# Kernel optimization log

Measured on AMD Instinct MI355X. Metric: run time of the kernel, lower is better.

The kernel has to match this reference:

```python
import jax, jax.numpy as jnp
import numpy as np

N_HEAD = 8
NORM_GROUPS = 32
EPS = 1e-6


def setup_inputs() -> dict:
    key = jax.random.key(0)
    ks = jax.random.split(key, 9)
    B, C, H, W, D = 1, 256, 16, 16, 16
    COND = 512
    x = jax.random.normal(ks[0], (B, C, H, W, D), dtype=jnp.float32)
    cond = jax.random.normal(ks[1], (B, COND), dtype=jnp.float32)
    # AdaGN linear scale/shift (torch Linear: weight [C, cond_dim], bias [C])
    w_scale = jax.random.normal(ks[2], (C, COND), dtype=jnp.float32) * 0.02
    b_scale = jax.random.normal(ks[3], (C,), dtype=jnp.float32) * 0.02
    w_shift = jax.random.normal(ks[4], (C, COND), dtype=jnp.float32) * 0.02
    b_shift = jax.random.normal(ks[5], (C,), dtype=jnp.float32) * 0.02
    # 1x1x1 conv3d weights collapse to matrices: qkv [3C, C] (no bias), out [C, C] + bias
    w_qkv = jax.random.normal(ks[6], (3 * C, C), dtype=jnp.float32) * (1.0 / np.sqrt(C))
    w_out = jax.random.normal(ks[7], (C, C), dtype=jnp.float32) * (1.0 / np.sqrt(C))
    b_out = jax.random.normal(ks[8], (C,), dtype=jnp.float32) * 0.02
    return {"x": x, "cond": cond, "w_scale": w_scale, "b_scale": b_scale,
            "w_shift": w_shift, "b_shift": b_shift, "w_qkv": w_qkv,
            "w_out": w_out, "b_out": b_out}


def _ada_gn(x, cond, w_scale, b_scale, w_shift, b_shift):
    B, C, H, W, D = x.shape
    G = NORM_GROUPS
    xg = x.reshape(B, G, C // G, H, W, D)
    mean = jnp.mean(xg, axis=(2, 3, 4, 5), keepdims=True)
    var = jnp.var(xg, axis=(2, 3, 4, 5), keepdims=True)
    x_norm = ((xg - mean) * jax.lax.rsqrt(var + EPS)).reshape(B, C, H, W, D)
    scale = (cond @ w_scale.T + b_scale)[:, :, None, None, None]  # [B,C,1,1,1]
    shift = (cond @ w_shift.T + b_shift)[:, :, None, None, None]
    return x_norm * (1.0 + scale) + shift


def reference(x, cond, w_scale, b_scale, w_shift, b_shift, w_qkv, w_out, b_out):
    B, C, H, W, D = x.shape
    nh = N_HEAD
    hd = C // nh
    N = H * W * D  # flattened spatial tokens
    norm = _ada_gn(x, cond, w_scale, b_scale, w_shift, b_shift)
    # 1x1x1 conv == channel matmul
    qkv = jnp.einsum('oc,bchwd->bohwd', w_qkv, norm)        # [B,3C,H,W,D]
    qkv = qkv.reshape(B, nh, 3 * hd, N)
    q, k, v = jnp.split(qkv, 3, axis=2)                      # each [B,nh,hd,N]
    attn = jnp.einsum('bnci,bncj->bnij', q, k) / jnp.sqrt(jnp.float32(C))
    attn = jax.nn.softmax(attn, axis=-1)                     # [B,nh,N,N]
    out = jnp.einsum('bnij,bncj->bnci', attn, v)             # [B,nh,hd,N]
    out = out.reshape(B, C, H, W, D)
    out = jnp.einsum('oc,bchwd->bohwd', w_out, out) + b_out[None, :, None, None, None]
    return out + x
```

## Files before the change

### kernel.cpp

```cpp
#include <hip/hip_runtime.h>
#include <math.h>

#define CCH 256
#define NN  4096
#define NHEAD 8
#define CONDD 512

typedef __attribute__((ext_vector_type(8))) short short8;
typedef __attribute__((ext_vector_type(4))) float f32x4;
typedef __attribute__((ext_vector_type(16))) float f32x16;

static __device__ __forceinline__ short f2bf(float f) {
    union { float f; uint32_t u; } v; v.f = f;
    uint32_t r = v.u + 0x7fffu + ((v.u >> 16) & 1u);
    return (short)(r >> 16);
}

static __device__ __forceinline__ uint32_t cvt_pk_bf16(float a, float b) {
    uint32_t r;
    asm("v_cvt_pk_bf16_f32 %0, %1, %2" : "=v"(r) : "v"(a), "v"(b));
    return r;
}

__global__ __launch_bounds__(256) void front_fused(const float* __restrict__ x,
                                                   const float* __restrict__ cond,
                                                   const float* __restrict__ w_scale,
                                                   const float* __restrict__ b_scale,
                                                   const float* __restrict__ w_shift,
                                                   const float* __restrict__ b_shift,
                                                   const float* __restrict__ wq,
                                                   const float* __restrict__ wo,
                                                   float* __restrict__ partial,
                                                   float* __restrict__ scale,
                                                   float* __restrict__ shift,
                                                   short* __restrict__ wqb,
                                                   short* __restrict__ wob) {
    __shared__ float rs[4], rss[4];
    int bb = blockIdx.x;
    int t = threadIdx.x;
    if (bb < 256) {
        const float4* p = (const float4*)(x + bb * 4096);
        float s = 0.f, ss = 0.f;
        for (int k = t; k < 1024; k += 256) {
            float4 v = p[k];
            s += v.x + v.y + v.z + v.w;
            ss += v.x * v.x + v.y * v.y + v.z * v.z + v.w * v.w;
        }
        #pragma unroll
        for (int off = 32; off; off >>= 1) { s += __shfl_xor(s, off); ss += __shfl_xor(ss, off); }
        int wid = t >> 6;
        if ((t & 63) == 0) { rs[wid] = s; rss[wid] = ss; }
        __syncthreads();
        if (t == 0) {
            partial[2 * bb] = rs[0] + rs[1] + rs[2] + rs[3];
            partial[2 * bb + 1] = rss[0] + rss[1] + rss[2] + rss[3];
        }
    } else if (bb < 1280) {
        int idx = (bb - 256) * 256 + t;
        if (idx < 196608) wqb[idx] = f2bf(wq[idx]);
        else              wob[idx - 196608] = f2bf(wo[idx - 196608]);
    } else {
        int o = (bb - 1280) * 4 + (t >> 6);
        int lane = t & 63;
        float ds = 0.f, dh = 0.f;
        for (int k = lane; k < CONDD; k += 64) {
            float cv = cond[k];
            ds += cv * w_scale[o * CONDD + k];
            dh += cv * w_shift[o * CONDD + k];
        }
        #pragma unroll
        for (int off = 32; off; off >>= 1) { ds += __shfl_xor(ds, off); dh += __shfl_xor(dh, off); }
        if (lane == 0) { scale[o] = ds + b_scale[o]; shift[o] = dh + b_shift[o]; }
    }
}

__global__ __launch_bounds__(256) void normalize_t(const float* __restrict__ x,
                                                   const float* __restrict__ partial,
                                                   const float* __restrict__ scale,
                                                   const float* __restrict__ shift,
                                                   short* __restrict__ norm_t) {
    __shared__ float gm[8], gr[8];
    __shared__ float Aa[64], Bb[64];
    __shared__ short tile[32 * 66];
    int i0 = blockIdx.x * 32;
    int c0 = blockIdx.y * 64;
    int g0 = c0 >> 3;
    int t = threadIdx.x;
    if (t < 8) {
        float s = 0.f, ss = 0.f;
        #pragma unroll
        for (int ch = 0; ch < 8; ++ch) {
            s += partial[((g0 + t) * 8 + ch) * 2];
            ss += partial[((g0 + t) * 8 + ch) * 2 + 1];
        }
        float mean = s * (1.0f / 32768.0f);
        float var = ss * (1.0f / 32768.0f) - mean * mean;
        gm[t] = mean;
        gr[t] = rsqrtf(var + 1e-6f);
    }
    __syncthreads();
    if (t < 64) {
        int c = c0 + t;
        float a = gr[t >> 3] * (1.0f + scale[c]);
        Aa[t] = a;
        Bb[t] = shift[c] - gm[t >> 3] * a;
    }
    __syncthreads();
    #pragma unroll
    for (int e0 = 0; e0 < 8; ++e0) {
        int e = e0 * 256 + t;
        int cl = e >> 5, il = e & 31;
        float v = x[(c0 + cl) * NN + i0 + il];
        tile[il * 66 + cl] = f2bf(v * Aa[cl] + Bb[cl]);
    }
    __syncthreads();
    #pragma unroll
    for (int e0 = 0; e0 < 4; ++e0) {
        int e = e0 * 256 + t;
        int il = e >> 5, cd = e & 31;
        uint32_t d = *(const uint32_t*)&tile[il * 66 + 2 * cd];
        *(uint32_t*)&norm_t[(i0 + il) * 256 + c0 + 2 * cd] = d;
    }
}

__global__ __launch_bounds__(256) void qkv_gemm(const short* __restrict__ wqb,
                                                const short* __restrict__ norm_t,
                                                short* __restrict__ qtb, short* __restrict__ ktb,
                                                short* __restrict__ vcb) {
    int t = threadIdx.x;
    int w = t >> 6, lane = t & 63, li = lane & 15, lg = lane >> 4;
    int o0 = blockIdx.x * 32;
    int i0 = blockIdx.y * 64 + w * 16;
    f32x4 acc[2] = {{0,0,0,0},{0,0,0,0}};
    const short* bbase = norm_t + (i0 + li) * 256 + 8 * lg;
    const short* abase = wqb + (o0 + li) * 256 + 8 * lg;
    #pragma unroll
    for (int ks = 0; ks < 8; ++ks) {
        short8 bfrag = *(const short8*)(bbase + ks * 32);
        #pragma unroll
        for (int f = 0; f < 2; ++f) {
            short8 afrag = *(const short8*)(abase + f * 16 * 256 + ks * 32);
            acc[f] = __builtin_amdgcn_mfma_f32_16x16x32_bf16(afrag, bfrag, acc[f], 0, 0, 0);
        }
    }
    int i = i0 + li;
    #pragma unroll
    for (int f = 0; f < 2; ++f) {
        #pragma unroll
        for (int r = 0; r < 4; ++r) {
            int o = o0 + 16 * f + 4 * lg + r;
            float v = acc[f][r];
            int h = o / 96;
            int rr = o - h * 96;
            int cc = rr & 31;
            int kind = rr >> 5;
            if (kind == 0)      qtb[(h * NN + i) * 32 + cc] = f2bf(v * (0.0625f * 1.44269504f));
            else if (kind == 1) ktb[(h * NN + i) * 32 + cc] = f2bf(v);
            else                vcb[(h * 32 + cc) * NN + i] = f2bf(v);
        }
    }
}

union PF { uint32_t u[4]; short8 s8; };

static __device__ __forceinline__ f32x16 qk_tile(short8 k0, short8 k1, short8 qf0, short8 qf1) {
    const f32x16 z = {0,0,0,0,0,0,0,0,0,0,0,0,0,0,0,0};
    __builtin_amdgcn_s_setprio(1);
    f32x16 s = __builtin_amdgcn_mfma_f32_32x32x16_bf16(k0, qf0, z, 0, 0, 0);
    s = __builtin_amdgcn_mfma_f32_32x32x16_bf16(k1, qf1, s, 0, 0, 0);
    __builtin_amdgcn_s_setprio(0);
    return s;
}

static __device__ __forceinline__ void pv_tile(f32x16 s, short8 v0, short8 v1,
                                               f32x16& acc, float& lsum) {
    float p[16];
    #pragma unroll
    for (int r = 0; r < 16; ++r) p[r] = __builtin_amdgcn_exp2f(s[r]);
    float u0 = 0.f, u1 = 0.f;
    #pragma unroll
    for (int r = 0; r < 4; ++r) { u0 += p[r] + p[4 + r]; u1 += p[8 + r] + p[12 + r]; }
    lsum += u0 + u1;
    auto A1 = __builtin_amdgcn_permlane32_swap(cvt_pk_bf16(p[0], p[1]),   cvt_pk_bf16(p[4], p[5]),   false, false);
    auto A2 = __builtin_amdgcn_permlane32_swap(cvt_pk_bf16(p[2], p[3]),   cvt_pk_bf16(p[6], p[7]),   false, false);
    auto A3 = __builtin_amdgcn_permlane32_swap(cvt_pk_bf16(p[8], p[9]),   cvt_pk_bf16(p[12], p[13]), false, false);
    auto A4 = __builtin_amdgcn_permlane32_swap(cvt_pk_bf16(p[10], p[11]), cvt_pk_bf16(p[14], p[15]), false, false);
    PF f1, f2;
    f1.u[0] = A1[0]; f1.u[1] = A2[0]; f1.u[2] = A1[1]; f1.u[3] = A2[1];
    f2.u[0] = A3[0]; f2.u[1] = A4[0]; f2.u[2] = A3[1]; f2.u[3] = A4[1];
    __builtin_amdgcn_s_setprio(1);
    acc = __builtin_amdgcn_mfma_f32_32x32x16_bf16(v0, f1.s8, acc, 0, 0, 0);
    acc = __builtin_amdgcn_mfma_f32_32x32x16_bf16(v1, f2.s8, acc, 0, 0, 0);
    __builtin_amdgcn_s_setprio(0);
}

__global__ __launch_bounds__(256, 4) void attention_mfma(const short* __restrict__ qtb,
                                                         const short* __restrict__ ktb,
                                                         const short* __restrict__ vcb,
                                                         short* __restrict__ attnT) {
    __shared__ float lds_acc[4][32][32];
    __shared__ float lds_lsum[4][32];

    int bid = blockIdx.x;
    int h = bid & 7;
    int i_base = (bid >> 3) * 32;
    int t = threadIdx.x;
    int w = t >> 6, lane = t & 63, l31 = lane & 31, hi = lane >> 5;

    const short* qrow = qtb + (h * NN + i_base + l31) * 32;
    short8 qf0 = *(const short8*)(qrow + 8 * hi);
    short8 qf1 = *(const short8*)(qrow + 16 + 8 * hi);

    const short* kbase = ktb + (h * NN + l31) * 32 + 8 * hi;
    const short* vrow  = vcb + (h * 32 + l31) * NN + 8 * hi;

    f32x16 acc = {0,0,0,0,0,0,0,0,0,0,0,0,0,0,0,0};
    float lsum = 0.f;

    int jstart = w * 1024;
    const short* kp = kbase + jstart * 32;
    const short* vp = vrow + jstart;

    short8 k0 = *(const short8*)kp, k1 = *(const short8*)(kp + 16);
    short8 v0 = *(const short8*)vp, v1 = *(const short8*)(vp + 16);
    f32x16 sA = qk_tile(k0, k1, qf0, qf1);
    kp += 1024; k0 = *(const short8*)kp; k1 = *(const short8*)(kp + 16);
    f32x16 sB;

    #pragma unroll 1
    for (int p = 0; p < 15; ++p) {
        sB = qk_tile(k0, k1, qf0, qf1);
        kp += 1024; k0 = *(const short8*)kp; k1 = *(const short8*)(kp + 16);
        pv_tile(sA, v0, v1, acc, lsum);
        vp += 32; v0 = *(const short8*)vp; v1 = *(const short8*)(vp + 16);

        sA = qk_tile(k0, k1, qf0, qf1);
        kp += 1024; k0 = *(const short8*)kp; k1 = *(const short8*)(kp + 16);
        pv_tile(sB, v0, v1, acc, lsum);
        vp += 32; v0 = *(const short8*)vp; v1 = *(const short8*)(vp + 16);
    }
    sB = qk_tile(k0, k1, qf0, qf1);
    pv_tile(sA, v0, v1, acc, lsum);
    vp += 32; v0 = *(const short8*)vp; v1 = *(const short8*)(vp + 16);
    pv_tile(sB, v0, v1, acc, lsum);

    lsum += __shfl_xor(lsum, 32);

    #pragma unroll
    for (int r = 0; r < 16; ++r) {
        int c = (r & 3) + 8 * (r >> 2) + 4 * hi;
        lds_acc[w][c][l31] = acc[r];
    }
    if (hi == 0) lds_lsum[w][l31] = lsum;
    __syncthreads();

    int q = t & 31, c0 = (t >> 5) * 4;
    float s0 = 0.f, s1 = 0.f, s2 = 0.f, s3 = 0.f, ls = 0.f;
    #pragma unroll
    for (int ww = 0; ww < 4; ++ww) {
        s0 += lds_acc[ww][c0 + 0][q];
        s1 += lds_acc[ww][c0 + 1][q];
        s2 += lds_acc[ww][c0 + 2][q];
        s3 += lds_acc[ww][c0 + 3][q];
        ls += lds_lsum[ww][q];
    }
    float inv = 1.0f / ls;
    uint2 uu;
    uu.x = cvt_pk_bf16(s0 * inv, s1 * inv);
    uu.y = cvt_pk_bf16(s2 * inv, s3 * inv);
    *(uint2*)&attnT[(i_base + q) * 256 + h * 32 + c0] = uu;
}

__global__ __launch_bounds__(256) void proj_gemm(const short* __restrict__ wob,
                                                 const short* __restrict__ attnT,
                                                 const float* __restrict__ b_out,
                                                 const float* __restrict__ x,
                                                 float* __restrict__ out) {
    int t = threadIdx.x;
    int w = t >> 6, lane = t & 63, li = lane & 15, lg = lane >> 4;
    int o0 = blockIdx.x * 32;
    int i0 = blockIdx.y * 64 + w * 16;
    f32x4 acc[2] = {{0,0,0,0},{0,0,0,0}};
    const short* bbase = attnT + (i0 + li) * 256 + 8 * lg;
    const short* abase = wob + (o0 + li) * 256 + 8 * lg;
    #pragma unroll
    for (int ks = 0; ks < 8; ++ks) {
        short8 bfrag = *(const short8*)(bbase + ks * 32);
        #pragma unroll
        for (int f = 0; f < 2; ++f) {
            short8 afrag = *(const short8*)(abase + f * 16 * 256 + ks * 32);
            acc[f] = __builtin_amdgcn_mfma_f32_16x16x32_bf16(afrag, bfrag, acc[f], 0, 0, 0);
        }
    }
    int i = i0 + li;
    #pragma unroll
    for (int f = 0; f < 2; ++f) {
        #pragma unroll
        for (int r = 0; r < 4; ++r) {
            int o = o0 + 16 * f + 4 * lg + r;
            out[o * NN + i] = acc[f][r] + b_out[o] + x[o * NN + i];
        }
    }
}

extern "C" void kernel_launch(void* const* d_in, const int* in_sizes, int n_in,
                              void* d_out, int out_size, void* d_ws, size_t ws_size,
                              hipStream_t stream) {
    const float* x       = (const float*)d_in[0];
    const float* cond    = (const float*)d_in[1];
    const float* w_scale = (const float*)d_in[2];
    const float* b_scale = (const float*)d_in[3];
    const float* w_shift = (const float*)d_in[4];
    const float* b_shift = (const float*)d_in[5];
    const float* w_qkv   = (const float*)d_in[6];
    const float* w_out   = (const float*)d_in[7];
    const float* b_out   = (const float*)d_in[8];
    float* out = (float*)d_out;

    float* ws = (float*)d_ws;
    float* scale   = ws;
    float* shift   = ws + 256;
    float* partial = ws + 512;
    short* norm_t = (short*)(ws + 1024);
    short* qtb = norm_t + 1048576;
    short* ktb = qtb + 1048576;
    short* vcb = ktb + 1048576;
    short* attnT = vcb + 1048576;
    short* wqb = attnT + 1048576;
    short* wob = wqb + 768 * 256;

    front_fused<<<1344, 256, 0, stream>>>(x, cond, w_scale, b_scale, w_shift, b_shift,
                                          w_qkv, w_out, partial, scale, shift, wqb, wob);
    normalize_t<<<dim3(128, 4), 256, 0, stream>>>(x, partial, scale, shift, norm_t);
    qkv_gemm<<<dim3(24, 64), 256, 0, stream>>>(wqb, norm_t, qtb, ktb, vcb);
    attention_mfma<<<1024, 256, 0, stream>>>(qtb, ktb, vcb, attnT);
    proj_gemm<<<dim3(8, 64), 256, 0, stream>>>(wob, attnT, b_out, x, out);
}
```

Before: 86.56 us.

## Split attention key range across eight waves and drop software pipelining

The attention block grows from 256 to 512 threads, so each of eight waves covers 512 keys instead of four waves covering 1024. The hand-written double-buffered QK/PV pipeline becomes a simple loop that loads K and V at the top of each iteration. The final LDS reduction now sums eight partials. The aim is to hide latency through more waves per CU rather than explicit software pipelining, at the cost of exposed load latency inside each wave and a larger cross-wave reduction.

```diff
diff --git a/kernel.cpp b/kernel.cpp
--- a/kernel.cpp
+++ b/kernel.cpp
@@ -161,45 +161,12 @@
     }
 }
 
-union PF { uint32_t u[4]; short8 s8; };
-
-static __device__ __forceinline__ f32x16 qk_tile(short8 k0, short8 k1, short8 qf0, short8 qf1) {
-    const f32x16 z = {0,0,0,0,0,0,0,0,0,0,0,0,0,0,0,0};
-    __builtin_amdgcn_s_setprio(1);
-    f32x16 s = __builtin_amdgcn_mfma_f32_32x32x16_bf16(k0, qf0, z, 0, 0, 0);
-    s = __builtin_amdgcn_mfma_f32_32x32x16_bf16(k1, qf1, s, 0, 0, 0);
-    __builtin_amdgcn_s_setprio(0);
-    return s;
-}
-
-static __device__ __forceinline__ void pv_tile(f32x16 s, short8 v0, short8 v1,
-                                               f32x16& acc, float& lsum) {
-    float p[16];
-    #pragma unroll
-    for (int r = 0; r < 16; ++r) p[r] = __builtin_amdgcn_exp2f(s[r]);
-    float u0 = 0.f, u1 = 0.f;
-    #pragma unroll
-    for (int r = 0; r < 4; ++r) { u0 += p[r] + p[4 + r]; u1 += p[8 + r] + p[12 + r]; }
-    lsum += u0 + u1;
-    auto A1 = __builtin_amdgcn_permlane32_swap(cvt_pk_bf16(p[0], p[1]),   cvt_pk_bf16(p[4], p[5]),   false, false);
-    auto A2 = __builtin_amdgcn_permlane32_swap(cvt_pk_bf16(p[2], p[3]),   cvt_pk_bf16(p[6], p[7]),   false, false);
-    auto A3 = __builtin_amdgcn_permlane32_swap(cvt_pk_bf16(p[8], p[9]),   cvt_pk_bf16(p[12], p[13]), false, false);
-    auto A4 = __builtin_amdgcn_permlane32_swap(cvt_pk_bf16(p[10], p[11]), cvt_pk_bf16(p[14], p[15]), false, false);
-    PF f1, f2;
-    f1.u[0] = A1[0]; f1.u[1] = A2[0]; f1.u[2] = A1[1]; f1.u[3] = A2[1];
-    f2.u[0] = A3[0]; f2.u[1] = A4[0]; f2.u[2] = A3[1]; f2.u[3] = A4[1];
-    __builtin_amdgcn_s_setprio(1);
-    acc = __builtin_amdgcn_mfma_f32_32x32x16_bf16(v0, f1.s8, acc, 0, 0, 0);
-    acc = __builtin_amdgcn_mfma_f32_32x32x16_bf16(v1, f2.s8, acc, 0, 0, 0);
-    __builtin_amdgcn_s_setprio(0);
-}
-
-__global__ __launch_bounds__(256, 4) void attention_mfma(const short* __restrict__ qtb,
+__global__ __launch_bounds__(512, 8) void attention_mfma(const short* __restrict__ qtb,
                                                          const short* __restrict__ ktb,
                                                          const short* __restrict__ vcb,
                                                          short* __restrict__ attnT) {
-    __shared__ float lds_acc[4][32][32];
-    __shared__ float lds_lsum[4][32];
+    __shared__ float lds_acc[8][32][32];
+    __shared__ float lds_lsum[8][32];
 
     int bid = blockIdx.x;
     int h = bid & 7;
@@ -211,38 +178,51 @@
     short8 qf0 = *(const short8*)(qrow + 8 * hi);
     short8 qf1 = *(const short8*)(qrow + 16 + 8 * hi);
 
-    const short* kbase = ktb + (h * NN + l31) * 32 + 8 * hi;
-    const short* vrow  = vcb + (h * 32 + l31) * NN + 8 * hi;
+    const short* kp = ktb + (h * NN + w * 512 + l31) * 32 + 8 * hi;
+    const short* vp = vcb + (h * 32 + l31) * NN + w * 512 + 8 * hi;
 
     f32x16 acc = {0,0,0,0,0,0,0,0,0,0,0,0,0,0,0,0};
+    const f32x16 zero16 = {0,0,0,0,0,0,0,0,0,0,0,0,0,0,0,0};
     float lsum = 0.f;
 
-    int jstart = w * 1024;
-    const short* kp = kbase + jstart * 32;
-    const short* vp = vrow + jstart;
-
-    short8 k0 = *(const short8*)kp, k1 = *(const short8*)(kp + 16);
-    short8 v0 = *(const short8*)vp, v1 = *(const short8*)(vp + 16);
-    f32x16 sA = qk_tile(k0, k1, qf0, qf1);
-    kp += 1024; k0 = *(const short8*)kp; k1 = *(const short8*)(kp + 16);
-    f32x16 sB;
-
     #pragma unroll 1
-    for (int p = 0; p < 15; ++p) {
-        sB = qk_tile(k0, k1, qf0, qf1);
-        kp += 1024; k0 = *(const short8*)kp; k1 = *(const short8*)(kp + 16);
-        pv_tile(sA, v0, v1, acc, lsum);
-        vp += 32; v0 = *(const short8*)vp; v1 = *(const short8*)(vp + 16);
-
-        sA = qk_tile(k0, k1, qf0, qf1);
-        kp += 1024; k0 = *(const short8*)kp; k1 = *(const short8*)(kp + 16);
-        pv_tile(sB, v0, v1, acc, lsum);
-        vp += 32; v0 = *(const short8*)vp; v1 = *(const short8*)(vp + 16);
-    }
-    sB = qk_tile(k0, k1, qf0, qf1);
-    pv_tile(sA, v0, v1, acc, lsum);
-    vp += 32; v0 = *(const short8*)vp; v1 = *(const short8*)(vp + 16);
-    pv_tile(sB, v0, v1, acc, lsum);
+    for (int tile = 0; tile < 16; ++tile) {
+        short8 k0 = *(const short8*)kp;
+        short8 k1 = *(const short8*)(kp + 16);
+        short8 v0 = *(const short8*)vp;
+        short8 v1 = *(const short8*)(vp + 16);
+        kp += 1024;
+        vp += 32;
+
+        __builtin_amdgcn_s_setprio(1);
+        f32x16 s = __builtin_amdgcn_mfma_f32_32x32x16_bf16(k0, qf0, zero16, 0, 0, 0);
+        s = __builtin_amdgcn_mfma_f32_32x32x16_bf16(k1, qf1, s, 0, 0, 0);
+        __builtin_amdgcn_s_setprio(0);
+
+        float p[16];
+        #pragma unroll
+        for (int r = 0; r < 16; ++r) p[r] = __builtin_amdgcn_exp2f(s[r]);
+
+        float u0 = 0.f, u1 = 0.f;
+        #pragma unroll
+        for (int r = 0; r < 4; ++r) { u0 += p[r] + p[4 + r]; u1 += p[8 + r] + p[12 + r]; }
+        lsum += u0 + u1;
+
+        auto A1 = __builtin_amdgcn_permlane32_swap(cvt_pk_bf16(p[0], p[1]),   cvt_pk_bf16(p[4], p[5]),   false, false);
+        auto A2 = __builtin_amdgcn_permlane32_swap(cvt_pk_bf16(p[2], p[3]),   cvt_pk_bf16(p[6], p[7]),   false, false);
+        auto A3 = __builtin_amdgcn_permlane32_swap(cvt_pk_bf16(p[8], p[9]),   cvt_pk_bf16(p[12], p[13]), false, false);
+        auto A4 = __builtin_amdgcn_permlane32_swap(cvt_pk_bf16(p[10], p[11]), cvt_pk_bf16(p[14], p[15]), false, false);
+
+        union PF { uint32_t u[4]; short8 s8; };
+        PF f1, f2;
+        f1.u[0] = A1[0]; f1.u[1] = A2[0]; f1.u[2] = A1[1]; f1.u[3] = A2[1];
+        f2.u[0] = A3[0]; f2.u[1] = A4[0]; f2.u[2] = A3[1]; f2.u[3] = A4[1];
+
+        __builtin_amdgcn_s_setprio(1);
+        acc = __builtin_amdgcn_mfma_f32_32x32x16_bf16(v0, f1.s8, acc, 0, 0, 0);
+        acc = __builtin_amdgcn_mfma_f32_32x32x16_bf16(v1, f2.s8, acc, 0, 0, 0);
+        __builtin_amdgcn_s_setprio(0);
+    }
 
     lsum += __shfl_xor(lsum, 32);
 
@@ -254,21 +234,23 @@
     if (hi == 0) lds_lsum[w][l31] = lsum;
     __syncthreads();
 
-    int q = t & 31, c0 = (t >> 5) * 4;
-    float s0 = 0.f, s1 = 0.f, s2 = 0.f, s3 = 0.f, ls = 0.f;
-    #pragma unroll
-    for (int ww = 0; ww < 4; ++ww) {
-        s0 += lds_acc[ww][c0 + 0][q];
-        s1 += lds_acc[ww][c0 + 1][q];
-        s2 += lds_acc[ww][c0 + 2][q];
-        s3 += lds_acc[ww][c0 + 3][q];
-        ls += lds_lsum[ww][q];
-    }
-    float inv = 1.0f / ls;
-    uint2 uu;
-    uu.x = cvt_pk_bf16(s0 * inv, s1 * inv);
-    uu.y = cvt_pk_bf16(s2 * inv, s3 * inv);
-    *(uint2*)&attnT[(i_base + q) * 256 + h * 32 + c0] = uu;
+    if (t < 256) {
+        int q = t & 31, c0 = (t >> 5) * 4;
+        float s0 = 0.f, s1 = 0.f, s2 = 0.f, s3 = 0.f, ls = 0.f;
+        #pragma unroll
+        for (int ww = 0; ww < 8; ++ww) {
+            s0 += lds_acc[ww][c0 + 0][q];
+            s1 += lds_acc[ww][c0 + 1][q];
+            s2 += lds_acc[ww][c0 + 2][q];
+            s3 += lds_acc[ww][c0 + 3][q];
+            ls += lds_lsum[ww][q];
+        }
+        float inv = 1.0f / ls;
+        uint2 uu;
+        uu.x = cvt_pk_bf16(s0 * inv, s1 * inv);
+        uu.y = cvt_pk_bf16(s2 * inv, s3 * inv);
+        *(uint2*)&attnT[(i_base + q) * 256 + h * 32 + c0] = uu;
+    }
 }
 
 __global__ __launch_bounds__(256) void proj_gemm(const short* __restrict__ wob,
@@ -333,6 +315,6 @@
                                           w_qkv, w_out, partial, scale, shift, wqb, wob);
     normalize_t<<<dim3(128, 4), 256, 0, stream>>>(x, partial, scale, shift, norm_t);
     qkv_gemm<<<dim3(24, 64), 256, 0, stream>>>(wqb, norm_t, qtb, ktb, vcb);
-    attention_mfma<<<1024, 256, 0, stream>>>(qtb, ktb, vcb, attnT);
+    attention_mfma<<<1024, 512, 0, stream>>>(qtb, ktb, vcb, attnT);
     proj_gemm<<<dim3(8, 64), 256, 0, stream>>>(wob, attnT, b_out, x, out);
 }
```

After: 102.0 us. +17.9%, slower.
